# Kernel tuning notes

Hardware: AMD Instinct MI355X
Metric: run time of the kernel (lower is better)

Reference implementation:

```python
import jax, jax.numpy as jnp
import numpy as np
import math

NUM_PARAM = 9
STRIDE = 1
BN_EPS = 1e-5


def _make_p_n(N):
    # matches LDConv._get_p_n: irregular kernel offset grid of N points
    base = round(math.sqrt(N))
    rows = N // base
    mod = N % base
    gx, gy = np.meshgrid(np.arange(rows), np.arange(base), indexing='ij')
    px, py = gx.ravel(), gy.ravel()
    if mod > 0:
        mx, my = np.meshgrid(np.arange(rows, rows + 1), np.arange(mod), indexing='ij')
        px = np.concatenate([px, mx.ravel()])
        py = np.concatenate([py, my.ravel()])
    return jnp.asarray(np.concatenate([px, py]), jnp.float32).reshape(1, 2 * N, 1, 1)


def _conv2d_same(x, w, stride, pad):
    return jax.lax.conv_general_dilated(
        x, w, (stride, stride), [(pad, pad), (pad, pad)],
        dimension_numbers=('NCHW', 'OIHW', 'NCHW'))


def _gather(xf, q, W, N):
    # xf: (b,c,H*W); q: (b,h,w,2N) int indices -> (b,c,h,w,N)
    idx = q[..., :N] * W + q[..., N:]
    return jax.vmap(lambda xb, ib: xb[:, ib])(xf, idx)


def setup_inputs() -> dict:
    key = jax.random.key(0)
    ks = jax.random.split(key, 3)
    B, C, H, W = 8, 128, 64, 64
    outc = 256
    x = jax.random.normal(ks[0], (B, C, H, W), jnp.float32)
    # p_conv init: uniform(-1e-4, 1e-4) weights, zero bias (per the torch module)
    p_conv_w = jax.random.uniform(ks[1], (2 * NUM_PARAM, C, 3, 3), jnp.float32, -1e-4, 1e-4)
    p_conv_b = jnp.zeros((2 * NUM_PARAM,), jnp.float32)
    conv_w = jax.random.normal(ks[2], (outc, C, NUM_PARAM, 1), jnp.float32) / math.sqrt(C * NUM_PARAM)
    bn_gamma = jnp.ones((outc,), jnp.float32)
    bn_beta = jnp.zeros((outc,), jnp.float32)
    bn_mean = jnp.zeros((outc,), jnp.float32)
    bn_var = jnp.ones((outc,), jnp.float32)
    return dict(x=x, p_conv_w=p_conv_w, p_conv_b=p_conv_b, conv_w=conv_w,
                bn_gamma=bn_gamma, bn_beta=bn_beta, bn_mean=bn_mean, bn_var=bn_var)


def reference(x, p_conv_w, p_conv_b, conv_w, bn_gamma, bn_beta, bn_mean, bn_var):
    N = NUM_PARAM
    B, C, H, W = x.shape
    offset = _conv2d_same(x, p_conv_w, STRIDE, 1) + p_conv_b[None, :, None, None]  # (b,2N,h,w)
    h, w = offset.shape[2], offset.shape[3]
    gx, gy = jnp.meshgrid(jnp.arange(0, h * STRIDE, STRIDE),
                          jnp.arange(0, w * STRIDE, STRIDE), indexing='ij')
    p_0 = jnp.concatenate([jnp.broadcast_to(gx, (1, N, h, w)),
                           jnp.broadcast_to(gy, (1, N, h, w))], axis=1).astype(x.dtype)
    p = (p_0 + _make_p_n(N) + offset).transpose(0, 2, 3, 1)  # (b,h,w,2N)

    q_lt = jnp.floor(jax.lax.stop_gradient(p))
    q_rb = q_lt + 1
    clampi = lambda q: jnp.concatenate([jnp.clip(q[..., :N], 0, H - 1),
                                        jnp.clip(q[..., N:], 0, W - 1)], -1).astype(jnp.int32)
    q_lt = clampi(q_lt)
    q_rb = clampi(q_rb)
    q_lb = jnp.concatenate([q_lt[..., :N], q_rb[..., N:]], -1)
    q_rt = jnp.concatenate([q_rb[..., :N], q_lt[..., N:]], -1)
    p = jnp.concatenate([jnp.clip(p[..., :N], 0, H - 1),
                         jnp.clip(p[..., N:], 0, W - 1)], -1)
    f = lambda q: q.astype(p.dtype)
    g_lt = (1 + (f(q_lt[..., :N]) - p[..., :N])) * (1 + (f(q_lt[..., N:]) - p[..., N:]))
    g_rb = (1 - (f(q_rb[..., :N]) - p[..., :N])) * (1 - (f(q_rb[..., N:]) - p[..., N:]))
    g_lb = (1 + (f(q_lb[..., :N]) - p[..., :N])) * (1 - (f(q_lb[..., N:]) - p[..., N:]))
    g_rt = (1 - (f(q_rt[..., :N]) - p[..., :N])) * (1 + (f(q_rt[..., N:]) - p[..., N:]))

    xf = x.reshape(B, C, H * W)
    x_off = (g_lt[:, None] * _gather(xf, q_lt, W, N)
             + g_rb[:, None] * _gather(xf, q_rb, W, N)
             + g_lb[:, None] * _gather(xf, q_lb, W, N)
             + g_rt[:, None] * _gather(xf, q_rt, W, N))  # (b,c,h,w,N)
    # rearrange 'b c h w n -> b c (h n) w'
    x_off = x_off.transpose(0, 1, 2, 4, 3).reshape(B, C, h * N, w)

    y = jax.lax.conv_general_dilated(x_off, conv_w, (N, 1), 'VALID',
                                     dimension_numbers=('NCHW', 'OIHW', 'NCHW'))
    scale = (bn_gamma / jnp.sqrt(bn_var + BN_EPS))[None, :, None, None]
    y = (y - bn_mean[None, :, None, None]) * scale + bn_beta[None, :, None, None]
    return y * jax.nn.sigmoid(y)  # SiLU
```

## Files before the change

kernel.cpp:

```cpp
#include <hip/hip_runtime.h>
#include <hip/hip_bf16.h>
#include <cstdint>

#define B_   8
#define C_   128
#define H_   64
#define W_   64
#define NPT  9
#define OC   256
#define K_   (C_*NPT)
#define HW   (H_*W_)

typedef __attribute__((ext_vector_type(8))) short short8;
typedef __attribute__((ext_vector_type(4))) float f32x4;
typedef __attribute__((ext_vector_type(4))) unsigned int u32x4;

static __device__ __forceinline__ unsigned short f2bf(float f) {
    union { float f; unsigned u; } a; a.f = f;
    unsigned r = a.u + 0x7fffu + ((a.u >> 16) & 1u);
    return (unsigned short)(r >> 16);
}
static __device__ __forceinline__ float bf2f(unsigned short u) {
    union { unsigned u; float f; } a; a.u = ((unsigned)u) << 16;
    return a.f;
}

__global__ __launch_bounds__(512) void k_offset2(const float* __restrict__ x,
                                                 const float* __restrict__ pw,
                                                 const float* __restrict__ pb,
                                                 float* __restrict__ off) {
    __shared__ __align__(16) float wlds[128 * 180];
    __shared__ float red[8 * 64 * 19];
    int b = blockIdx.x >> 5;
    int i0 = (blockIdx.x & 31) * 2;
    int t = threadIdx.x;

    for (int idx = t; idx < 128 * 9 * 18; idx += 512) {
        int c = idx / 162;
        int r = idx - c * 162;
        int tap = r / 18;
        int o = r - tap * 18;
        wlds[c * 180 + tap * 20 + o] = pw[o * K_ + c * 9 + tap];
    }
    __syncthreads();

    int j = t & 63;
    int cg = t >> 6;
    const float* xb = x + (size_t)b * C_ * HW;
    float acc[2][18];
#pragma unroll
    for (int p = 0; p < 2; ++p)
#pragma unroll
        for (int o = 0; o < 18; ++o) acc[p][o] = 0.f;

    for (int cc = 0; cc < 16; ++cc) {
        int c = cg * 16 + cc;
        const float* xc = xb + (size_t)c * HW;
        float xv[4][3];
#pragma unroll
        for (int q = 0; q < 4; ++q) {
            int row = i0 - 1 + q;
            if (row >= 0 && row < H_) {
                const float* xr = xc + row * W_;
                xv[q][1] = xr[j];
                xv[q][0] = (j > 0)  ? xr[j - 1] : 0.f;
                xv[q][2] = (j < 63) ? xr[j + 1] : 0.f;
            } else {
                xv[q][0] = xv[q][1] = xv[q][2] = 0.f;
            }
        }
        const float* wc = wlds + c * 180;
#pragma unroll
        for (int tap = 0; tap < 9; ++tap) {
            const int kh = tap / 3, kw = tap % 3;
            float w18[20];
            *(f32x4*)(w18 + 0)  = *(const f32x4*)(wc + tap * 20 + 0);
            *(f32x4*)(w18 + 4)  = *(const f32x4*)(wc + tap * 20 + 4);
            *(f32x4*)(w18 + 8)  = *(const f32x4*)(wc + tap * 20 + 8);
            *(f32x4*)(w18 + 12) = *(const f32x4*)(wc + tap * 20 + 12);
            *(f32x4*)(w18 + 16) = *(const f32x4*)(wc + tap * 20 + 16);
#pragma unroll
            for (int p = 0; p < 2; ++p) {
                float xval = xv[p + kh][kw];
#pragma unroll
                for (int o = 0; o < 18; ++o) acc[p][o] += w18[o] * xval;
            }
        }
    }

#pragma unroll
    for (int p = 0; p < 2; ++p) {
        __syncthreads();
#pragma unroll
        for (int o = 0; o < 18; ++o) red[(cg * 64 + j) * 19 + o] = acc[p][o];
        __syncthreads();
        for (int e = t; e < 64 * 18; e += 512) {
            int jj = e / 18, o = e - jj * 18;
            float s = 0.f;
#pragma unroll
            for (int g = 0; g < 8; ++g) s += red[(g * 64 + jj) * 19 + o];
            off[(((size_t)b * 18 + o) * H_ + (i0 + p)) * W_ + jj] = s + pb[o];
        }
    }
}

__global__ __launch_bounds__(256) void k_prepw(const float* __restrict__ cw,
                                               const float* __restrict__ gam,
                                               const float* __restrict__ bet,
                                               const float* __restrict__ mu,
                                               const float* __restrict__ var,
                                               unsigned short* __restrict__ wbf,
                                               float* __restrict__ bias) {
    int idx = blockIdx.x * 256 + threadIdx.x;
    int oc = idx / K_;
    int r = idx - oc * K_;
    int n = r >> 7;
    int c = r & 127;
    float sc = gam[oc] * rsqrtf(var[oc] + 1e-5f);
    wbf[idx] = f2bf(cw[oc * K_ + c * NPT + n] * sc);
    if (blockIdx.x == 0 && threadIdx.x < OC) {
        int o = threadIdx.x;
        float s = gam[o] * rsqrtf(var[o] + 1e-5f);
        bias[o] = bet[o] - mu[o] * s;
    }
}

__global__ __launch_bounds__(256) void k_transpose(const float* __restrict__ x,
                                                   unsigned short* __restrict__ xT) {
    __shared__ float sp[128][65];
    int b = blockIdx.x >> 6, i = blockIdx.x & 63;
    int t = threadIdx.x;
    const float* xb = x + (size_t)b * C_ * HW + i * 64;
#pragma unroll
    for (int it = 0; it < 8; ++it) {
        int q = it * 256 + t;
        int c = q >> 4, j4 = q & 15;
        f32x4 v = *(const f32x4*)(xb + (size_t)c * HW + j4 * 4);
        *(f32x4*)&sp[c][j4 * 4] = v;
    }
    __syncthreads();
    unsigned short* xo = xT + ((size_t)b * HW + i * 64) * C_;
#pragma unroll
    for (int it = 0; it < 4; ++it) {
        int q = it * 256 + t;
        int j = q >> 4, cg = q & 15;
        u32x4 pk;
#pragma unroll
        for (int p2 = 0; p2 < 4; ++p2) {
            pk[p2] = (uint32_t)f2bf(sp[cg * 8 + p2 * 2][j])
                   | ((uint32_t)f2bf(sp[cg * 8 + p2 * 2 + 1][j]) << 16);
        }
        *(u32x4*)(xo + (size_t)j * C_ + cg * 8) = pk;
    }
}

__global__ __launch_bounds__(512, 4) void k_fused(const unsigned short* __restrict__ xT,
                                                  const float* __restrict__ off,
                                                  const unsigned short* __restrict__ wbf,
                                                  const float* __restrict__ bias,
                                                  float* __restrict__ out) {
    __shared__ __align__(16) char smem[70144];
    int bid = blockIdx.x;
    int wg = (bid & 7) * 64 + (bid >> 3);
    int b = wg >> 6;
    int i = wg & 63;
    int tid = threadIdx.x;
    int wv = tid >> 6, lane = tid & 63, j = lane;
    int lrow = lane & 15, lg = lane >> 4;
    const unsigned short* xTb = xT + (size_t)b * HW * C_;
    const char* Bb = (const char*)wbf;
    float* soff = (float*)(smem + 65536);

    auto stageB = [&](int buf, int hs) {
        char* base = smem + 16384 + buf * 16384;
#pragma unroll
        for (int q = 0; q < 2; ++q) {
            int ch = q * 512 + tid;
            int row = ch >> 2, slot = ch & 3;
            int src = row * 2304 + hs * 64 + ((slot ^ (row & 3)) * 16);
            __builtin_amdgcn_global_load_lds(
                (const __attribute__((address_space(1))) uint32_t*)(Bb + src),
                (__attribute__((address_space(3))) uint32_t*)(base + ch * 16), 16, 0, 0);
        }
    };

    short8 tp0, tp1, tp2, tp3;
    float w00, w11, w01, w10;
    auto gather_issue = [&](int kt) {
        int n = kt >> 1;
        int c8 = (kt & 1) * 8 + wv;
        float ox = soff[n * 64 + j];
        float oy = soff[(n + 9) * 64 + j];
        float pxf = (float)(i + n / 3) + ox;
        float pyf = (float)(j + n % 3) + oy;
        float fx = floorf(pxf), fy = floorf(pyf);
        int r0 = max(0, min(63, (int)fx));
        int r1 = max(0, min(63, (int)fx + 1));
        int c0 = max(0, min(63, (int)fy));
        int c1 = max(0, min(63, (int)fy + 1));
        float pxc = fminf(fmaxf(pxf, 0.f), 63.f);
        float pyc = fminf(fmaxf(pyf, 0.f), 63.f);
        float ax = 1.f + ((float)r0 - pxc);
        float bx = 1.f - ((float)r1 - pxc);
        float ay = 1.f + ((float)c0 - pyc);
        float by = 1.f - ((float)c1 - pyc);
        w00 = ax * ay; w11 = bx * by; w01 = ax * by; w10 = bx * ay;
        const unsigned short* g = xTb + c8 * 8;
        tp0 = *(const short8*)(g + (size_t)(r0 * 64 + c0) * C_);
        tp1 = *(const short8*)(g + (size_t)(r1 * 64 + c1) * C_);
        tp2 = *(const short8*)(g + (size_t)(r0 * 64 + c1) * C_);
        tp3 = *(const short8*)(g + (size_t)(r1 * 64 + c0) * C_);
    };
    auto bilinear_write = [&](int kt) {
        u32x4 pk;
#pragma unroll
        for (int p2 = 0; p2 < 4; ++p2) {
            unsigned short rr[2];
#pragma unroll
            for (int e = 0; e < 2; ++e) {
                int ei = p2 * 2 + e;
                float v = w00 * bf2f((unsigned short)tp0[ei])
                        + w11 * bf2f((unsigned short)tp1[ei])
                        + w01 * bf2f((unsigned short)tp2[ei])
                        + w10 * bf2f((unsigned short)tp3[ei]);
                rr[e] = f2bf(v);
            }
            pk[p2] = (uint32_t)rr[0] | ((uint32_t)rr[1] << 16);
        }
        *(u32x4*)(smem + (kt & 1) * 8192 + wv * 1024 + j * 16) = pk;
    };

    f32x4 zero = {0.f, 0.f, 0.f, 0.f};
    f32x4 acc[4][2];
#pragma unroll
    for (int m = 0; m < 4; ++m)
#pragma unroll
        for (int n = 0; n < 2; ++n) acc[m][n] = zero;

    auto compute_half = [&](int abuf, int bbuf, int h) {
        const char* sa = smem + abuf * 8192;
        const char* sb = smem + 16384 + bbuf * 16384;
        short8 afr[4], bfr[2];
#pragma unroll
        for (int m = 0; m < 4; ++m)
            afr[m] = *(const short8*)(sa + (h * 4 + lg) * 1024 + (m * 16 + lrow) * 16);
#pragma unroll
        for (int n = 0; n < 2; ++n) {
            int row = wv * 32 + n * 16 + lrow;
            bfr[n] = *(const short8*)(sb + row * 64 + ((lg ^ (row & 3)) * 16));
        }
#pragma unroll
        for (int m = 0; m < 4; ++m)
#pragma unroll
            for (int n = 0; n < 2; ++n)
                acc[m][n] = __builtin_amdgcn_mfma_f32_16x16x32_bf16(afr[m], bfr[n], acc[m][n], 0, 0, 0);
    };

    for (int e = tid; e < 1152; e += 512) {
        int plane = e >> 6, jj = e & 63;
        soff[e] = off[(((size_t)b * 18 + plane) * H_ + i) * W_ + jj];
    }
    stageB(0, 0);
    stageB(1, 1);
    __syncthreads();
    gather_issue(0);
    bilinear_write(0);
    stageB(2, 2);
    __syncthreads();

#pragma unroll 6
    for (int kt = 0; kt < 18; ++kt) {
        const int hs0 = 2 * kt;
        if (hs0 + 2 < 36) stageB((hs0 + 2) % 3, hs0 + 2);
        if (kt < 17) gather_issue(kt + 1);
        compute_half(kt & 1, hs0 % 3, 0);
        __syncthreads();
        if (hs0 + 3 < 36) stageB((hs0 + 3) % 3, hs0 + 3);
        if (kt < 17) bilinear_write(kt + 1);
        compute_half(kt & 1, (hs0 + 1) % 3, 1);
        __syncthreads();
    }

#pragma unroll
    for (int n = 0; n < 2; ++n) {
        int oc = wv * 32 + n * 16 + lrow;
        float bs = bias[oc];
#pragma unroll
        for (int m = 0; m < 4; ++m) {
#pragma unroll
            for (int r = 0; r < 4; ++r) {
                int px = m * 16 + lg * 4 + r;
                float v = acc[m][n][r] + bs;
                float sv = v / (1.f + __expf(-v));
                out[((size_t)b * OC + oc) * HW + i * 64 + px] = sv;
            }
        }
    }
}

extern "C" void kernel_launch(void* const* d_in, const int* in_sizes, int n_in,
                              void* d_out, int out_size, void* d_ws, size_t ws_size,
                              hipStream_t stream) {
    const float* x   = (const float*)d_in[0];
    const float* pw  = (const float*)d_in[1];
    const float* pb  = (const float*)d_in[2];
    const float* cw  = (const float*)d_in[3];
    const float* gam = (const float*)d_in[4];
    const float* bet = (const float*)d_in[5];
    const float* mu  = (const float*)d_in[6];
    const float* var = (const float*)d_in[7];
    float* out = (float*)d_out;

    char* ws = (char*)d_ws;
    float* off           = (float*)ws;
    unsigned short* wbf  = (unsigned short*)(ws + 2359296);
    float* bias          = (float*)(ws + 2949120);
    unsigned short* xT   = (unsigned short*)(ws + 2950144);

    hipLaunchKernelGGL(k_offset2,   dim3(256),  dim3(512), 0, stream, x, pw, pb, off);
    hipLaunchKernelGGL(k_prepw,     dim3(1152), dim3(256), 0, stream, cw, gam, bet, mu, var, wbf, bias);
    hipLaunchKernelGGL(k_transpose, dim3(512),  dim3(256), 0, stream, x, xT);
    hipLaunchKernelGGL(k_fused,     dim3(512),  dim3(512), 0, stream, xT, off, wbf, bias, out);
}
```

Baseline: 101.5 us.

## Compute offset conv as split-bf16 MFMA implicit GEMM over padded NHWC input

Replaces the scalar FP32 3x3 offset convolution with an implicit GEMM on bf16 MFMA. Inputs and weights are split into hi/lo bf16 pairs and combined with four MFMAs to keep near-FP32 accuracy. A new transpose kernel writes a zero-padded NHWC hi/lo copy of x, and a border-zeroing kernel fills the padding. Tiles are staged via global_load_lds with XOR-swizzled LDS. This trades the scalar FMA work for three extra small launches, an extra pass over x, and MFMA work padded from 18 to 32 output channels.

```diff
diff --git a/kernel.cpp b/kernel.cpp
--- a/kernel.cpp
+++ b/kernel.cpp
@@ -10,6 +10,7 @@
 #define OC   256
 #define K_   (C_*NPT)
 #define HW   (H_*W_)
+#define XTPB 557568
 
 typedef __attribute__((ext_vector_type(8))) short short8;
 typedef __attribute__((ext_vector_type(4))) float f32x4;
@@ -25,81 +26,166 @@
     return a.f;
 }
 
-__global__ __launch_bounds__(512) void k_offset2(const float* __restrict__ x,
-                                                 const float* __restrict__ pw,
-                                                 const float* __restrict__ pb,
-                                                 float* __restrict__ off) {
-    __shared__ __align__(16) float wlds[128 * 180];
-    __shared__ float red[8 * 64 * 19];
-    int b = blockIdx.x >> 5;
-    int i0 = (blockIdx.x & 31) * 2;
+__global__ __launch_bounds__(256) void k_zerob(unsigned short* __restrict__ xh,
+                                               unsigned short* __restrict__ xl) {
+    int idx = blockIdx.x * 256 + threadIdx.x;
+    if (idx >= 8 * 33280) return;
+    int b = idx / 33280, pos = idx - b * 33280;
+    int addr;
+    if (pos < 8448) addr = pos;
+    else if (pos < 16896) addr = 65 * 66 * 128 + (pos - 8448);
+    else if (pos < 25088) { int r = 1 + (pos - 16896) / 128, ch = (pos - 16896) % 128; addr = r * 66 * 128 + ch; }
+    else                  { int r = 1 + (pos - 25088) / 128, ch = (pos - 25088) % 128; addr = (r * 66 + 65) * 128 + ch; }
+    xh[(size_t)b * XTPB + addr] = 0;
+    xl[(size_t)b * XTPB + addr] = 0;
+}
+
+__global__ __launch_bounds__(256) void k_transpose2(const float* __restrict__ x,
+                                                    unsigned short* __restrict__ xh,
+                                                    unsigned short* __restrict__ xl) {
+    __shared__ float sp[128][65];
+    int b = blockIdx.x >> 6, i = blockIdx.x & 63;
     int t = threadIdx.x;
-
-    for (int idx = t; idx < 128 * 9 * 18; idx += 512) {
-        int c = idx / 162;
-        int r = idx - c * 162;
-        int tap = r / 18;
-        int o = r - tap * 18;
-        wlds[c * 180 + tap * 20 + o] = pw[o * K_ + c * 9 + tap];
+    const float* xb = x + (size_t)b * C_ * HW + i * 64;
+#pragma unroll
+    for (int it = 0; it < 8; ++it) {
+        int q = it * 256 + t;
+        int c = q >> 4, j4 = q & 15;
+        *(f32x4*)&sp[c][j4 * 4] = *(const f32x4*)(xb + (size_t)c * HW + j4 * 4);
     }
     __syncthreads();
-
-    int j = t & 63;
-    int cg = t >> 6;
-    const float* xb = x + (size_t)b * C_ * HW;
-    float acc[2][18];
-#pragma unroll
-    for (int p = 0; p < 2; ++p)
-#pragma unroll
-        for (int o = 0; o < 18; ++o) acc[p][o] = 0.f;
-
-    for (int cc = 0; cc < 16; ++cc) {
-        int c = cg * 16 + cc;
-        const float* xc = xb + (size_t)c * HW;
-        float xv[4][3];
-#pragma unroll
-        for (int q = 0; q < 4; ++q) {
-            int row = i0 - 1 + q;
-            if (row >= 0 && row < H_) {
-                const float* xr = xc + row * W_;
-                xv[q][1] = xr[j];
-                xv[q][0] = (j > 0)  ? xr[j - 1] : 0.f;
-                xv[q][2] = (j < 63) ? xr[j + 1] : 0.f;
-            } else {
-                xv[q][0] = xv[q][1] = xv[q][2] = 0.f;
+    size_t obase = (size_t)b * XTPB + ((size_t)(i + 1) * 66 + 1) * 128;
+#pragma unroll
+    for (int it = 0; it < 4; ++it) {
+        int q = it * 256 + t;
+        int j = q >> 4, cg = q & 15;
+        u32x4 ph, pl;
+#pragma unroll
+        for (int p2 = 0; p2 < 4; ++p2) {
+            float a = sp[cg * 8 + p2 * 2][j];
+            float bb = sp[cg * 8 + p2 * 2 + 1][j];
+            unsigned short ah = f2bf(a), bh = f2bf(bb);
+            unsigned short al = f2bf(a - bf2f(ah)), bl = f2bf(bb - bf2f(bh));
+            ph[p2] = (uint32_t)ah | ((uint32_t)bh << 16);
+            pl[p2] = (uint32_t)al | ((uint32_t)bl << 16);
+        }
+        *(u32x4*)(xh + obase + (size_t)j * 128 + cg * 8) = ph;
+        *(u32x4*)(xl + obase + (size_t)j * 128 + cg * 8) = pl;
+    }
+}
+
+__global__ __launch_bounds__(256) void k_prepow2(const float* __restrict__ pw,
+                                                 unsigned short* __restrict__ wh,
+                                                 unsigned short* __restrict__ wl) {
+    int idx = blockIdx.x * 256 + threadIdx.x;
+    int o = idx / 1152, kp = idx - o * 1152;
+    int tp = kp >> 7, c = kp & 127;
+    float v = (o < 18) ? pw[o * K_ + c * 9 + tp] : 0.f;
+    unsigned short hi = f2bf(v);
+    unsigned short lo = f2bf(v - bf2f(hi));
+    int db = (o * 2304 + tp * 256 + ((c * 2) ^ ((o & 7) << 4))) >> 1;
+    wh[db] = hi;
+    wl[db] = lo;
+}
+
+__global__ __launch_bounds__(256) void k_offgemm2(const unsigned short* __restrict__ xh,
+                                                  const unsigned short* __restrict__ xl,
+                                                  const unsigned short* __restrict__ wh,
+                                                  const unsigned short* __restrict__ wl,
+                                                  const float* __restrict__ pb,
+                                                  float* __restrict__ off) {
+    __shared__ __align__(16) char smem[81920];
+    int bid = blockIdx.x;
+    int wg = (bid & 7) * 32 + (bid >> 3);
+    int b = wg >> 5;
+    int i0 = (wg & 31) * 2;
+    int tid = threadIdx.x;
+    int wv = tid >> 6, lane = tid & 63;
+    int lrow = lane & 15, lg = lane >> 4;
+    const char* xhb = (const char*)(xh + (size_t)b * XTPB);
+    const char* xlb = (const char*)(xl + (size_t)b * XTPB);
+    const char* whb = (const char*)wh;
+    const char* wlb = (const char*)wl;
+
+    f32x4 zero = {0.f, 0.f, 0.f, 0.f};
+    f32x4 acc[2][2];
+#pragma unroll
+    for (int m = 0; m < 2; ++m)
+#pragma unroll
+        for (int n = 0; n < 2; ++n) acc[m][n] = zero;
+
+    for (int tpt = 0; tpt < 9; ++tpt) {
+        int dh = tpt / 3 - 1, dw = tpt % 3 - 1;
+#pragma unroll
+        for (int q = 0; q < 8; ++q) {
+            int ch = q * 256 + tid;
+            int row = ch >> 4, slot = ch & 15;
+            int ri = i0 + (row >> 6) + dh + 1;
+            int ci = (row & 63) + dw + 1;
+            int src = (ri * 66 + ci) * 256 + ((slot * 16) ^ ((row & 7) << 4));
+            __builtin_amdgcn_global_load_lds(
+                (const __attribute__((address_space(1))) uint32_t*)(xhb + src),
+                (__attribute__((address_space(3))) uint32_t*)(smem + ch * 16), 16, 0, 0);
+            __builtin_amdgcn_global_load_lds(
+                (const __attribute__((address_space(1))) uint32_t*)(xlb + src),
+                (__attribute__((address_space(3))) uint32_t*)(smem + 32768 + ch * 16), 16, 0, 0);
+        }
+#pragma unroll
+        for (int q = 0; q < 2; ++q) {
+            int ch = q * 256 + tid;
+            int row = ch >> 4, slot = ch & 15;
+            int src = row * 2304 + tpt * 256 + slot * 16;
+            __builtin_amdgcn_global_load_lds(
+                (const __attribute__((address_space(1))) uint32_t*)(whb + src),
+                (__attribute__((address_space(3))) uint32_t*)(smem + 65536 + ch * 16), 16, 0, 0);
+            __builtin_amdgcn_global_load_lds(
+                (const __attribute__((address_space(1))) uint32_t*)(wlb + src),
+                (__attribute__((address_space(3))) uint32_t*)(smem + 73728 + ch * 16), 16, 0, 0);
+        }
+        __syncthreads();
+#pragma unroll
+        for (int ks = 0; ks < 4; ++ks) {
+            short8 ah[2], al[2], bh[2], bl[2];
+#pragma unroll
+            for (int m = 0; m < 2; ++m) {
+                int row = wv * 32 + m * 16 + lrow;
+                int byt = (ks * 64 + lg * 16) ^ ((row & 7) << 4);
+                ah[m] = *(const short8*)(smem + row * 256 + byt);
+                al[m] = *(const short8*)(smem + 32768 + row * 256 + byt);
             }
-        }
-        const float* wc = wlds + c * 180;
-#pragma unroll
-        for (int tap = 0; tap < 9; ++tap) {
-            const int kh = tap / 3, kw = tap % 3;
-            float w18[20];
-            *(f32x4*)(w18 + 0)  = *(const f32x4*)(wc + tap * 20 + 0);
-            *(f32x4*)(w18 + 4)  = *(const f32x4*)(wc + tap * 20 + 4);
-            *(f32x4*)(w18 + 8)  = *(const f32x4*)(wc + tap * 20 + 8);
-            *(f32x4*)(w18 + 12) = *(const f32x4*)(wc + tap * 20 + 12);
-            *(f32x4*)(w18 + 16) = *(const f32x4*)(wc + tap * 20 + 16);
-#pragma unroll
-            for (int p = 0; p < 2; ++p) {
-                float xval = xv[p + kh][kw];
-#pragma unroll
-                for (int o = 0; o < 18; ++o) acc[p][o] += w18[o] * xval;
+#pragma unroll
+            for (int n = 0; n < 2; ++n) {
+                int row = n * 16 + lrow;
+                int byt = (ks * 64 + lg * 16) ^ ((row & 7) << 4);
+                bh[n] = *(const short8*)(smem + 65536 + row * 256 + byt);
+                bl[n] = *(const short8*)(smem + 73728 + row * 256 + byt);
             }
-        }
-    }
-
-#pragma unroll
-    for (int p = 0; p < 2; ++p) {
+#pragma unroll
+            for (int m = 0; m < 2; ++m)
+#pragma unroll
+                for (int n = 0; n < 2; ++n) {
+                    acc[m][n] = __builtin_amdgcn_mfma_f32_16x16x32_bf16(ah[m], bh[n], acc[m][n], 0, 0, 0);
+                    acc[m][n] = __builtin_amdgcn_mfma_f32_16x16x32_bf16(ah[m], bl[n], acc[m][n], 0, 0, 0);
+                    acc[m][n] = __builtin_amdgcn_mfma_f32_16x16x32_bf16(al[m], bh[n], acc[m][n], 0, 0, 0);
+                    acc[m][n] = __builtin_amdgcn_mfma_f32_16x16x32_bf16(al[m], bl[n], acc[m][n], 0, 0, 0);
+                }
+        }
         __syncthreads();
-#pragma unroll
-        for (int o = 0; o < 18; ++o) red[(cg * 64 + j) * 19 + o] = acc[p][o];
-        __syncthreads();
-        for (int e = t; e < 64 * 18; e += 512) {
-            int jj = e / 18, o = e - jj * 18;
-            float s = 0.f;
-#pragma unroll
-            for (int g = 0; g < 8; ++g) s += red[(g * 64 + jj) * 19 + o];
-            off[(((size_t)b * 18 + o) * H_ + (i0 + p)) * W_ + jj] = s + pb[o];
+    }
+#pragma unroll
+    for (int n = 0; n < 2; ++n) {
+        int oc = n * 16 + lrow;
+        if (oc < 18) {
+            float bs = pb[oc];
+#pragma unroll
+            for (int m = 0; m < 2; ++m) {
+#pragma unroll
+                for (int r = 0; r < 4; ++r) {
+                    int px = wv * 32 + m * 16 + lg * 4 + r;
+                    int ii = i0 + (px >> 6), jj = px & 63;
+                    off[(((size_t)b * 18 + oc) * H_ + ii) * W_ + jj] = acc[m][n][r] + bs;
+                }
+            }
         }
     }
 }
@@ -316,9 +402,16 @@
     unsigned short* wbf  = (unsigned short*)(ws + 2359296);
     float* bias          = (float*)(ws + 2949120);
     unsigned short* xT   = (unsigned short*)(ws + 2950144);
-
-    hipLaunchKernelGGL(k_offset2,   dim3(256),  dim3(512), 0, stream, x, pw, pb, off);
-    hipLaunchKernelGGL(k_prepw,     dim3(1152), dim3(256), 0, stream, cw, gam, bet, mu, var, wbf, bias);
-    hipLaunchKernelGGL(k_transpose, dim3(512),  dim3(256), 0, stream, x, xT);
-    hipLaunchKernelGGL(k_fused,     dim3(512),  dim3(512), 0, stream, xT, off, wbf, bias, out);
-}
+    unsigned short* whi  = (unsigned short*)(ws + 11338752);
+    unsigned short* wlo  = (unsigned short*)(ws + 11412480);
+    unsigned short* xh   = (unsigned short*)(ws + 11486208);
+    unsigned short* xl   = (unsigned short*)(ws + 20407296);
+
+    hipLaunchKernelGGL(k_zerob,      dim3(1040), dim3(256), 0, stream, xh, xl);
+    hipLaunchKernelGGL(k_transpose2, dim3(512),  dim3(256), 0, stream, x, xh, xl);
+    hipLaunchKernelGGL(k_prepow2,    dim3(144),  dim3(256), 0, stream, pw, whi, wlo);
+    hipLaunchKernelGGL(k_prepw,      dim3(1152), dim3(256), 0, stream, cw, gam, bet, mu, var, wbf, bias);
+    hipLaunchKernelGGL(k_transpose,  dim3(512),  dim3(256), 0, stream, x, xT);
+    hipLaunchKernelGGL(k_offgemm2,   dim3(256),  dim3(256), 0, stream, xh, xl, whi, wlo, pb, off);
+    hipLaunchKernelGGL(k_fused,      dim3(512),  dim3(512), 0, stream, xT, off, wbf, bias, out);
+}
```

Result: slower. 106.2 us (+4.7%).
